# Kernel optimization log

Measured on AMD Instinct MI355X. Metric: run time of the kernel, lower is better.

The kernel has to match this reference:

```python
import jax, jax.numpy as jnp
import numpy as np
import math

EARTH_RADIUS_KM = 6371.0
D_MAX_KM = 200.0
K_D = 64

B, N, D, R = 64, 128, 128, 4096


def setup_inputs() -> dict:
    key = jax.random.key(0)
    ks = jax.random.split(key, 7)
    S = jax.random.normal(ks[0], (B, N, D), dtype=jnp.float32)
    region_emb = jax.random.normal(ks[1], (R, D), dtype=jnp.float32)
    traj_lat = jax.random.uniform(ks[2], (B, N), dtype=jnp.float32)
    traj_lon = jax.random.uniform(ks[3], (B, N), dtype=jnp.float32)
    region_centroids = jax.random.uniform(ks[4], (R, 2), dtype=jnp.float32)
    key_padding_mask = jax.random.randint(ks[5], (B, N), 0, 2).astype(bool)
    E_d_match = jax.random.normal(ks[6], (K_D,), dtype=jnp.float32) * 0.1
    return {"S": S, "region_emb": region_emb, "traj_lat": traj_lat,
            "traj_lon": traj_lon, "region_centroids": region_centroids,
            "key_padding_mask": key_padding_mask, "E_d_match": E_d_match}


def _haversine_km(lat1, lon1, lat2, lon2):
    deg2rad = math.pi / 180.0
    lat1r = lat1 * deg2rad
    lat2r = lat2 * deg2rad
    dlat = (lat2 - lat1) * deg2rad
    dlon = (lon2 - lon1) * deg2rad
    a = jnp.sin(dlat / 2) ** 2 + jnp.cos(lat1r) * jnp.cos(lat2r) * jnp.sin(dlon / 2) ** 2
    a = jnp.clip(a, 0.0, 1.0)
    return EARTH_RADIUS_KM * 2.0 * jnp.arcsin(jnp.sqrt(a))


def _interp_scalar(table, x):
    K = table.shape[0]
    x = jnp.clip(x, 0.0, K - 1 - 1e-06)
    k = jnp.floor(x).astype(jnp.int32)
    frac = x - k.astype(x.dtype)
    lo = table[k]
    hi = table[jnp.minimum(k + 1, K - 1)]
    return (1.0 - frac) * lo + frac * hi


def reference(S, region_emb, traj_lat, traj_lon, region_centroids,
              key_padding_mask, E_d_match):
    Dm = S.shape[-1]
    cand_lat = region_centroids[:, 0]  # [R]
    cand_lon = region_centroids[:, 1]
    # [B, n, R] pairwise distance trajectory-position <-> region centroid
    dd = _haversine_km(traj_lat[:, :, None], traj_lon[:, :, None],
                       cand_lat[None, None, :], cand_lon[None, None, :])
    d_bin = jnp.clip(dd, 0.0, D_MAX_KM) / D_MAX_KM * (K_D - 1)
    bias_match = _interp_scalar(E_d_match, d_bin)  # [B, n, R]
    scores = jnp.einsum('bnd,rd->bnr', S, region_emb) / math.sqrt(Dm)
    scores = scores + bias_match
    mask = key_padding_mask[:, :, None]  # [B, n, 1]
    scores = jnp.where(mask, -jnp.inf, scores)
    attn = jnp.nan_to_num(jax.nn.softmax(scores, axis=1), nan=0.0)
    scores_safe = jnp.where(mask, 0.0, scores)
    return (attn * scores_safe).sum(axis=1)  # [B, R]
```

## Files before the change

### kernel.cpp

```cpp
#include <hip/hip_runtime.h>
#include <math.h>

#define BB 64
#define NN 128
#define DD 128
#define RR 4096
#define KD 64

typedef _Float16 f16x8 __attribute__((ext_vector_type(8)));
typedef _Float16 f16x4 __attribute__((ext_vector_type(4)));
typedef float    float4v __attribute__((ext_vector_type(4)));

#define WS_S_OFF (RR * DD)

__global__ __launch_bounds__(256)
void convert_kernel(const float* __restrict__ S, const float* __restrict__ E,
                    _Float16* __restrict__ ws) {
    int i = blockIdx.x * 256 + threadIdx.x;
    const int NE4 = (RR * DD) / 4;
    if (i < NE4) {
        float4 v = ((const float4*)E)[i];
        f16x4 h = {(_Float16)v.x, (_Float16)v.y, (_Float16)v.z, (_Float16)v.w};
        ((f16x4*)ws)[i] = h;
    } else {
        int j = i - NE4;
        float4 v = ((const float4*)S)[j];
        f16x4 h = {(_Float16)v.x, (_Float16)v.y, (_Float16)v.z, (_Float16)v.w};
        ((f16x4*)(ws + WS_S_OFF))[j] = h;
    }
}

__global__ __launch_bounds__(256, 5)
void matching_kernel(const _Float16* __restrict__ wsE,
                     const _Float16* __restrict__ wsS,
                     const float* __restrict__ tlat,
                     const float* __restrict__ tlon,
                     const float* __restrict__ cent,
                     const int*   __restrict__ kpm,
                     const float* __restrict__ Etab,
                     float* __restrict__ out)
{
    __shared__ _Float16 ldsB[2][64 * 32];
    __shared__ float colLatX[64], colLonX[64], colCos[64];
    __shared__ float rowLatX[128], rowLonX[128], rowCn[128];
    __shared__ float2 tab2[KD];
    __shared__ int   idx[128];
    __shared__ unsigned long long smask[2];
    __shared__ float pe[4][64], pw[4][64];

    const int tid = threadIdx.x;
    const int b  = blockIdx.y;
    const int r0 = blockIdx.x * 64;
    const int wv = tid >> 6, lane = tid & 63;
    const int lrow = lane & 15, quad = lane >> 4;

    const float D2R    = 0.017453292519943295f;
    const float HSC    = 0.008726646259971648f * 4013.73f;
    const float L2E    = 1.4426950408889634f;
    const float SCALE2 = 0.08838834764831845f * 1.4426950408889634f;
    const float LN2    = 0.6931471805599453f;

    const int srow = tid >> 2, scth = tid & 3;
    const _Float16* gB = wsE + (size_t)(r0 + srow) * DD + scth * 8;
    uint4 creg = *(const uint4*)gB;

    if (tid < 128) {
        bool valid = (kpm[b * NN + tid] == 0);
        unsigned long long m = __ballot(valid);
        if (lane == 0) smask[wv] = m;
    } else if (tid < 128 + KD) {
        int k = tid - 128;
        float lo = Etab[k];
        float hi = Etab[k < KD - 1 ? k + 1 : KD - 1];
        tab2[k] = make_float2(lo * L2E, (hi - lo) * L2E);
    } else {
        int c = tid - 192, r = r0 + c;
        float cla = cent[2 * r], clo = cent[2 * r + 1];
        colLatX[c] = cla * HSC; colLonX[c] = clo * HSC;
        colCos[c]  = cosf(cla * D2R);
    }
    __syncthreads();

    const unsigned long long m0 = smask[0], m1 = smask[1];
    const int c0 = __popcll(m0);
    const int V  = c0 + __popcll(m1);
    const int Mt = (V + 15) >> 4;

    if (tid < 128) {
        unsigned long long mw = (tid < 64) ? m0 : m1;
        int ln = tid & 63;
        if ((mw >> ln) & 1ull) {
            int pos = __popcll(mw & ((1ull << ln) - 1ull)) + (tid < 64 ? 0 : c0);
            idx[pos] = tid;
        }
    }
    __syncthreads();

    if (tid < 128) {
        if (tid < V) {
            int n = idx[tid];
            float la = tlat[b * NN + n], lo = tlon[b * NN + n];
            rowLatX[tid] = la * HSC; rowLonX[tid] = lo * HSC;
            rowCn[tid]   = cosf(la * D2R);
        } else { rowLatX[tid] = 0.0f; rowLonX[tid] = 0.0f; rowCn[tid] = -1.0f; }
    }

    const bool t0a = (wv < Mt), t1a = (wv + 4) < Mt;
    int rc0 = wv * 16 + lrow, rc1 = (wv + 4) * 16 + lrow;
    const _Float16* pA0 = wsS + (size_t)(b * NN + idx[(rc0 < V ? rc0 : V - 1)]) * DD;
    const _Float16* pA1 = wsS + (size_t)(b * NN + idx[(rc1 < V ? rc1 : V - 1)]) * DD;

    float4v acc[2][4] = {};
    const int sslot = (scth ^ (srow & 3)) * 8;
#pragma unroll
    for (int kk = 0; kk < 4; ++kk) {
        *(uint4*)&ldsB[kk & 1][srow * 32 + sslot] = creg;
        if (kk < 3) creg = *(const uint4*)(gB + (kk + 1) * 32);
        f16x8 af0, af1;
        if (t0a) af0 = *(const f16x8*)(pA0 + kk * 32 + quad * 8);
        if (t1a) af1 = *(const f16x8*)(pA1 + kk * 32 + quad * 8);
        __syncthreads();
#pragma unroll
        for (int tr = 0; tr < 4; ++tr) {
            int row = tr * 16 + lrow;
            f16x8 bb = *(const f16x8*)&ldsB[kk & 1][row * 32 + ((quad ^ (row & 3)) * 8)];
            if (t0a) acc[0][tr] = __builtin_amdgcn_mfma_f32_16x16x32_f16(af0, bb, acc[0][tr], 0, 0, 0);
            if (t1a) acc[1][tr] = __builtin_amdgcn_mfma_f32_16x16x32_f16(af1, bb, acc[1][tr], 0, 0, 0);
        }
    }

    float tlX[8], toX[8], cn8[8];
#pragma unroll
    for (int i = 0; i < 2; ++i)
#pragma unroll
        for (int e = 0; e < 4; ++e) {
            int n = (wv + 4 * i) * 16 + quad * 4 + e;
            int j = i * 4 + e;
            tlX[j] = rowLatX[n]; toX[j] = rowLonX[n]; cn8[j] = rowCn[n];
        }

#pragma unroll
    for (int tr = 0; tr < 4; ++tr) {
        int col = tr * 16 + lrow;
        float claX = colLatX[col], cloX = colLonX[col], cc = colCos[col];
        float es = 0.0f, ws2 = 0.0f;
#pragma unroll
        for (int i = 0; i < 2; ++i) {
            if (i == 0 ? !t0a : !t1a) continue;
#pragma unroll
            for (int e = 0; e < 4; ++e) {
                int j = i * 4 + e;
                float hd = claX - tlX[j];
                float ho = cloX - toX[j];
                float a  = fmaf(hd, hd, (cn8[j] * cc) * (ho * ho));
                float x  = fminf(__builtin_amdgcn_sqrtf(a), 62.999996f);
                int   k  = (int)x;
                float fr = x - (float)k;
                float2 te = tab2[k];
                float bias2 = fmaf(fr, te.y, te.x);
                float s2 = fmaf(acc[i][tr][e], SCALE2, bias2);
                float ex = __builtin_amdgcn_exp2f(s2);
                ex = (cn8[j] < 0.0f) ? 0.0f : ex;
                es += ex;
                ws2 = fmaf(ex, s2, ws2);
            }
        }
        es  += __shfl_xor(es, 16, 64);  es  += __shfl_xor(es, 32, 64);
        ws2 += __shfl_xor(ws2, 16, 64); ws2 += __shfl_xor(ws2, 32, 64);
        if (lane < 16) { pe[wv][col] = es; pw[wv][col] = ws2; }
    }
    __syncthreads();

    if (tid < 64) {
        float es = pe[0][tid] + pe[1][tid] + pe[2][tid] + pe[3][tid];
        float ws = pw[0][tid] + pw[1][tid] + pw[2][tid] + pw[3][tid];
        float o = es > 0.0f ? (ws / es) * LN2 : 0.0f;
        out[(size_t)b * RR + r0 + tid] = o;
    }
}

extern "C" void kernel_launch(void* const* d_in, const int* in_sizes, int n_in,
                              void* d_out, int out_size, void* d_ws, size_t ws_size,
                              hipStream_t stream) {
    const float* S    = (const float*)d_in[0];
    const float* Remb = (const float*)d_in[1];
    const float* tlat = (const float*)d_in[2];
    const float* tlon = (const float*)d_in[3];
    const float* cent = (const float*)d_in[4];
    const int*   kpm  = (const int*)d_in[5];
    const float* Etab = (const float*)d_in[6];
    float* out = (float*)d_out;
    _Float16* ws = (_Float16*)d_ws;

    convert_kernel<<<1536, 256, 0, stream>>>(S, Remb, ws);

    dim3 grid(RR / 64, BB, 1);
    matching_kernel<<<grid, dim3(256, 1, 1), 0, stream>>>(
        ws, ws + WS_S_OFF, tlat, tlon, cent, kpm, Etab, out);
}
```

Before: 89.99 us.

## Move mask compaction and geometry precompute into prep kernel; single-stage LDS GEMM

The prep kernel now builds the compacted valid-row index, converts only valid S rows to fp16 in compacted order, and precomputes per-region and per-row geometry plus the bias table into workspace. The matching kernel then loads the full 64x128 region-embedding tile into LDS in one shot and preloads all A fragments, removing three barriers and the redundant per-block mask, cos and table work. This trades larger LDS use (occupancy hint lowered to 4) for fewer syncs and less repeated setup across the 4096 blocks.

Result: no change. 91.52 us (+1.7%).

```diff
diff --git a/kernel.cpp b/kernel.cpp
--- a/kernel.cpp
+++ b/kernel.cpp
@@ -11,41 +11,92 @@
 typedef _Float16 f16x4 __attribute__((ext_vector_type(4)));
 typedef float    float4v __attribute__((ext_vector_type(4)));
 
-#define WS_S_OFF (RR * DD)
+#define WS_E_OFF   0
+#define WS_S_OFF   (1048576)
+#define WS_CG_OFF  (3145728)
+#define WS_RG_OFF  (3145728 + 65536)
+#define WS_TAB_OFF (3145728 + 65536 + 131072)
+#define WS_V_OFF   (3145728 + 65536 + 131072 + 512)
+
+#define D2R_C    0.017453292519943295f
+#define HSC_C    (0.008726646259971648f * 4013.73f)
+#define L2E_C    1.4426950408889634f
+#define SCALE2_C (0.08838834764831845f * 1.4426950408889634f)
+#define LN2_C    0.6931471805599453f
 
 __global__ __launch_bounds__(256)
-void convert_kernel(const float* __restrict__ S, const float* __restrict__ E,
-                    _Float16* __restrict__ ws) {
-    int i = blockIdx.x * 256 + threadIdx.x;
-    const int NE4 = (RR * DD) / 4;
-    if (i < NE4) {
+void prep_kernel(const float* __restrict__ S, const float* __restrict__ E,
+                 const float* __restrict__ tlat, const float* __restrict__ tlon,
+                 const float* __restrict__ cent, const int* __restrict__ kpm,
+                 const float* __restrict__ Etab, char* __restrict__ wsb) {
+    const int blk = blockIdx.x, tid = threadIdx.x;
+    if (blk < 512) {
+        int i = blk * 256 + tid;
         float4 v = ((const float4*)E)[i];
         f16x4 h = {(_Float16)v.x, (_Float16)v.y, (_Float16)v.z, (_Float16)v.w};
-        ((f16x4*)ws)[i] = h;
+        ((f16x4*)(wsb + WS_E_OFF))[i] = h;
+    } else if (blk < 528) {
+        int r = (blk - 512) * 256 + tid;
+        float cla = cent[2 * r], clo = cent[2 * r + 1];
+        ((float4*)(wsb + WS_CG_OFF))[r] =
+            make_float4(cla * HSC_C, clo * HSC_C, cosf(cla * D2R_C), 0.0f);
+    } else if (blk == 528) {
+        if (tid < KD) {
+            float lo = Etab[tid];
+            float hi = Etab[tid < KD - 1 ? tid + 1 : KD - 1];
+            ((float2*)(wsb + WS_TAB_OFF))[tid] =
+                make_float2(lo * L2E_C, (hi - lo) * L2E_C);
+        }
     } else {
-        int j = i - NE4;
-        float4 v = ((const float4*)S)[j];
-        f16x4 h = {(_Float16)v.x, (_Float16)v.y, (_Float16)v.z, (_Float16)v.w};
-        ((f16x4*)(ws + WS_S_OFF))[j] = h;
+        __shared__ int idx[128];
+        __shared__ unsigned long long smask[2];
+        const int b = blk - 529;
+        const int wv = tid >> 6, lane = tid & 63;
+        if (tid < 128) {
+            bool valid = (kpm[b * NN + tid] == 0);
+            unsigned long long m = __ballot(valid);
+            if (lane == 0) smask[wv] = m;
+        }
+        __syncthreads();
+        const unsigned long long m0 = smask[0], m1 = smask[1];
+        const int c0 = __popcll(m0);
+        const int V  = c0 + __popcll(m1);
+        if (tid == 0) ((int*)(wsb + WS_V_OFF))[b] = V;
+        if (tid < 128) {
+            unsigned long long mw = (tid < 64) ? m0 : m1;
+            int ln = tid & 63;
+            if ((mw >> ln) & 1ull) {
+                int pos = __popcll(mw & ((1ull << ln) - 1ull)) + (tid < 64 ? 0 : c0);
+                idx[pos] = tid;
+            }
+        }
+        __syncthreads();
+        if (tid < 128) {
+            float4 rg;
+            if (tid < V) {
+                int n = idx[tid];
+                float la = tlat[b * NN + n], lo = tlon[b * NN + n];
+                rg = make_float4(la * HSC_C, lo * HSC_C, cosf(la * D2R_C), 0.0f);
+            } else rg = make_float4(0.0f, 0.0f, -1.0f, 0.0f);
+            ((float4*)(wsb + WS_RG_OFF))[b * 128 + tid] = rg;
+        }
+        f16x4* dst = (f16x4*)(wsb + WS_S_OFF) + (size_t)b * NN * (DD / 4);
+        const float4* src = (const float4*)S + (size_t)b * NN * (DD / 4);
+        for (int ch = tid; ch < V * 32; ch += 256) {
+            int row = ch >> 5, cp = ch & 31;
+            float4 v = src[idx[row] * 32 + cp];
+            f16x4 h = {(_Float16)v.x, (_Float16)v.y, (_Float16)v.z, (_Float16)v.w};
+            dst[row * 32 + cp] = h;
+        }
     }
 }
 
-__global__ __launch_bounds__(256, 5)
-void matching_kernel(const _Float16* __restrict__ wsE,
-                     const _Float16* __restrict__ wsS,
-                     const float* __restrict__ tlat,
-                     const float* __restrict__ tlon,
-                     const float* __restrict__ cent,
-                     const int*   __restrict__ kpm,
-                     const float* __restrict__ Etab,
-                     float* __restrict__ out)
-{
-    __shared__ _Float16 ldsB[2][64 * 32];
+__global__ __launch_bounds__(256, 4)
+void matching_kernel(const char* __restrict__ wsb, float* __restrict__ out) {
+    __shared__ _Float16 ldsE[64 * 128];
     __shared__ float colLatX[64], colLonX[64], colCos[64];
     __shared__ float rowLatX[128], rowLonX[128], rowCn[128];
     __shared__ float2 tab2[KD];
-    __shared__ int   idx[128];
-    __shared__ unsigned long long smask[2];
     __shared__ float pe[4][64], pw[4][64];
 
     const int tid = threadIdx.x;
@@ -54,78 +105,54 @@
     const int wv = tid >> 6, lane = tid & 63;
     const int lrow = lane & 15, quad = lane >> 4;
 
-    const float D2R    = 0.017453292519943295f;
-    const float HSC    = 0.008726646259971648f * 4013.73f;
-    const float L2E    = 1.4426950408889634f;
-    const float SCALE2 = 0.08838834764831845f * 1.4426950408889634f;
-    const float LN2    = 0.6931471805599453f;
-
-    const int srow = tid >> 2, scth = tid & 3;
-    const _Float16* gB = wsE + (size_t)(r0 + srow) * DD + scth * 8;
-    uint4 creg = *(const uint4*)gB;
-
-    if (tid < 128) {
-        bool valid = (kpm[b * NN + tid] == 0);
-        unsigned long long m = __ballot(valid);
-        if (lane == 0) smask[wv] = m;
-    } else if (tid < 128 + KD) {
-        int k = tid - 128;
-        float lo = Etab[k];
-        float hi = Etab[k < KD - 1 ? k + 1 : KD - 1];
-        tab2[k] = make_float2(lo * L2E, (hi - lo) * L2E);
-    } else {
-        int c = tid - 192, r = r0 + c;
-        float cla = cent[2 * r], clo = cent[2 * r + 1];
-        colLatX[c] = cla * HSC; colLonX[c] = clo * HSC;
-        colCos[c]  = cosf(cla * D2R);
-    }
+    const _Float16* wsE = (const _Float16*)(wsb + WS_E_OFF);
+    const _Float16* wsS = (const _Float16*)(wsb + WS_S_OFF);
+
+    const int V  = ((const int*)(wsb + WS_V_OFF))[b];
+    const int Mt = (V + 15) >> 4;
+    const bool t0a = (wv < Mt), t1a = (wv + 4) < Mt;
+
+    uint4 creg[4];
+    int srowv[4], scv[4];
+#pragma unroll
+    for (int t = 0; t < 4; ++t) {
+        int i = tid + t * 256;
+        srowv[t] = i >> 4; scv[t] = i & 15;
+        creg[t] = *(const uint4*)(wsE + (size_t)(r0 + srowv[t]) * DD + scv[t] * 8);
+    }
+    float4 cg, rg; float2 t2;
+    if (tid < 64)        cg = ((const float4*)(wsb + WS_CG_OFF))[r0 + tid];
+    else if (tid < 128)  t2 = ((const float2*)(wsb + WS_TAB_OFF))[tid - 64];
+    else                 rg = ((const float4*)(wsb + WS_RG_OFF))[b * 128 + (tid - 128)];
+
+    int rc0 = wv * 16 + lrow, rc1 = (wv + 4) * 16 + lrow;
+    const _Float16* pA0 = wsS + (size_t)(b * NN + (rc0 < V ? rc0 : 0)) * DD;
+    const _Float16* pA1 = wsS + (size_t)(b * NN + (rc1 < V ? rc1 : 0)) * DD;
+    f16x8 af0[4], af1[4];
+#pragma unroll
+    for (int kk = 0; kk < 4; ++kk) {
+        if (t0a) af0[kk] = *(const f16x8*)(pA0 + kk * 32 + quad * 8);
+        if (t1a) af1[kk] = *(const f16x8*)(pA1 + kk * 32 + quad * 8);
+    }
+
+#pragma unroll
+    for (int t = 0; t < 4; ++t)
+        *(uint4*)&ldsE[srowv[t] * DD + ((scv[t] ^ (srowv[t] & 7)) * 8)] = creg[t];
+    if (tid < 64) { colLatX[tid] = cg.x; colLonX[tid] = cg.y; colCos[tid] = cg.z; }
+    else if (tid < 128) tab2[tid - 64] = t2;
+    else { int n = tid - 128; rowLatX[n] = rg.x; rowLonX[n] = rg.y; rowCn[n] = rg.z; }
     __syncthreads();
 
-    const unsigned long long m0 = smask[0], m1 = smask[1];
-    const int c0 = __popcll(m0);
-    const int V  = c0 + __popcll(m1);
-    const int Mt = (V + 15) >> 4;
-
-    if (tid < 128) {
-        unsigned long long mw = (tid < 64) ? m0 : m1;
-        int ln = tid & 63;
-        if ((mw >> ln) & 1ull) {
-            int pos = __popcll(mw & ((1ull << ln) - 1ull)) + (tid < 64 ? 0 : c0);
-            idx[pos] = tid;
-        }
-    }
-    __syncthreads();
-
-    if (tid < 128) {
-        if (tid < V) {
-            int n = idx[tid];
-            float la = tlat[b * NN + n], lo = tlon[b * NN + n];
-            rowLatX[tid] = la * HSC; rowLonX[tid] = lo * HSC;
-            rowCn[tid]   = cosf(la * D2R);
-        } else { rowLatX[tid] = 0.0f; rowLonX[tid] = 0.0f; rowCn[tid] = -1.0f; }
-    }
-
-    const bool t0a = (wv < Mt), t1a = (wv + 4) < Mt;
-    int rc0 = wv * 16 + lrow, rc1 = (wv + 4) * 16 + lrow;
-    const _Float16* pA0 = wsS + (size_t)(b * NN + idx[(rc0 < V ? rc0 : V - 1)]) * DD;
-    const _Float16* pA1 = wsS + (size_t)(b * NN + idx[(rc1 < V ? rc1 : V - 1)]) * DD;
-
     float4v acc[2][4] = {};
-    const int sslot = (scth ^ (srow & 3)) * 8;
 #pragma unroll
     for (int kk = 0; kk < 4; ++kk) {
-        *(uint4*)&ldsB[kk & 1][srow * 32 + sslot] = creg;
-        if (kk < 3) creg = *(const uint4*)(gB + (kk + 1) * 32);
-        f16x8 af0, af1;
-        if (t0a) af0 = *(const f16x8*)(pA0 + kk * 32 + quad * 8);
-        if (t1a) af1 = *(const f16x8*)(pA1 + kk * 32 + quad * 8);
-        __syncthreads();
 #pragma unroll
         for (int tr = 0; tr < 4; ++tr) {
             int row = tr * 16 + lrow;
-            f16x8 bb = *(const f16x8*)&ldsB[kk & 1][row * 32 + ((quad ^ (row & 3)) * 8)];
-            if (t0a) acc[0][tr] = __builtin_amdgcn_mfma_f32_16x16x32_f16(af0, bb, acc[0][tr], 0, 0, 0);
-            if (t1a) acc[1][tr] = __builtin_amdgcn_mfma_f32_16x16x32_f16(af1, bb, acc[1][tr], 0, 0, 0);
+            int c = kk * 4 + quad;
+            f16x8 bb = *(const f16x8*)&ldsE[row * DD + ((c ^ (lrow & 7)) * 8)];
+            if (t0a) acc[0][tr] = __builtin_amdgcn_mfma_f32_16x16x32_f16(af0[kk], bb, acc[0][tr], 0, 0, 0);
+            if (t1a) acc[1][tr] = __builtin_amdgcn_mfma_f32_16x16x32_f16(af1[kk], bb, acc[1][tr], 0, 0, 0);
         }
     }
 
@@ -158,7 +185,7 @@
                 float fr = x - (float)k;
                 float2 te = tab2[k];
                 float bias2 = fmaf(fr, te.y, te.x);
-                float s2 = fmaf(acc[i][tr][e], SCALE2, bias2);
+                float s2 = fmaf(acc[i][tr][e], SCALE2_C, bias2);
                 float ex = __builtin_amdgcn_exp2f(s2);
                 ex = (cn8[j] < 0.0f) ? 0.0f : ex;
                 es += ex;
@@ -174,7 +201,7 @@
     if (tid < 64) {
         float es = pe[0][tid] + pe[1][tid] + pe[2][tid] + pe[3][tid];
         float ws = pw[0][tid] + pw[1][tid] + pw[2][tid] + pw[3][tid];
-        float o = es > 0.0f ? (ws / es) * LN2 : 0.0f;
+        float o = es > 0.0f ? (ws / es) * LN2_C : 0.0f;
         out[(size_t)b * RR + r0 + tid] = o;
     }
 }
@@ -190,11 +217,10 @@
     const int*   kpm  = (const int*)d_in[5];
     const float* Etab = (const float*)d_in[6];
     float* out = (float*)d_out;
-    _Float16* ws = (_Float16*)d_ws;
-
-    convert_kernel<<<1536, 256, 0, stream>>>(S, Remb, ws);
+    char* wsb = (char*)d_ws;
+
+    prep_kernel<<<593, 256, 0, stream>>>(S, Remb, tlat, tlon, cent, kpm, Etab, wsb);
 
     dim3 grid(RR / 64, BB, 1);
-    matching_kernel<<<grid, dim3(256, 1, 1), 0, stream>>>(
-        ws, ws + WS_S_OFF, tlat, tlon, cent, kpm, Etab, out);
+    matching_kernel<<<grid, dim3(256, 1, 1), 0, stream>>>(wsb, out);
 }
```
